# Optimization experiments

Measured on AMD Instinct MI355X. Metric: run time of the kernel, lower is better.

The kernel has to match this reference:

```python
import jax, jax.numpy as jnp
import numpy as np
from jax import lax

E = 4      # n_experts
K = 2      # top_k
D = 1024   # d_model
B, S = 4, 4096


def setup_inputs() -> dict:
    key = jax.random.key(0)
    ks = jax.random.split(key, 9)
    sc = 1.0 / np.sqrt(D)
    x = jax.random.normal(ks[0], (B, S, D), dtype=jnp.float32)
    Wg = jax.random.normal(ks[1], (E, D, D), dtype=jnp.float32) * sc
    bg = jax.random.normal(ks[2], (E, D), dtype=jnp.float32) * sc
    Wv = jax.random.normal(ks[3], (E, D, D), dtype=jnp.float32) * sc
    bv = jax.random.normal(ks[4], (E, D), dtype=jnp.float32) * sc
    Wd = jax.random.normal(ks[5], (E, D, D), dtype=jnp.float32) * sc
    # decay_bias_init = 1.0 (torch init.constant_)
    bd = jnp.ones((E, D), dtype=jnp.float32)
    Wgate = jax.random.normal(ks[7], (E, D), dtype=jnp.float32) * sc
    return {"x": x, "Wg": Wg, "bg": bg, "Wv": Wv, "bv": bv,
            "Wd": Wd, "bd": bd, "Wgate": Wgate}


def reference(x, Wg, bg, Wv, bv, Wd, bd, Wgate):
    # Per-expert projections (torch Linear: y = x @ W.T + b; W is (out,in))
    g = jnp.einsum('bsd,eod->ebso', x, Wg) + bg[:, None, None, :]  # (E,B,S,D)
    v = jnp.einsum('bsd,eod->ebso', x, Wv) + bv[:, None, None, :]
    d = jnp.einsum('bsd,eod->ebso', x, Wd) + bd[:, None, None, :]
    x_scan = jax.nn.sigmoid(g) * jnp.tanh(v)
    a = 0.001 + 0.998 * jax.nn.sigmoid(d)

    # Causal linear RNN: h_t = a_t * h_{t-1} + x_t, vectorized over (E,B,D)
    xs = jnp.moveaxis(x_scan, 2, 0)  # (S,E,B,D)
    as_ = jnp.moveaxis(a, 2, 0)      # (S,E,B,D)

    def step(h, inp):
        a_t, x_t = inp
        h = a_t * h + x_t
        return h, h

    h0 = jnp.zeros((E, B, x.shape[-1]), dtype=x.dtype)
    _, outs = lax.scan(step, h0, (as_, xs))        # (S,E,B,D)
    expert_outs = jnp.transpose(outs, (2, 0, 3, 1))  # (B,S,D,E)

    # Router: top-k experts per token, softmax over selected logits
    gate_logits = jnp.einsum('bsd,ed->bse', x, Wgate)  # (B,S,E)
    top_vals, top_idx = lax.top_k(gate_logits, K)      # (B,S,K)
    weights = jax.nn.softmax(top_vals, axis=-1)        # (B,S,K)

    idx = jnp.broadcast_to(top_idx[:, :, None, :],
                           (x.shape[0], x.shape[1], x.shape[2], K))
    selected = jnp.take_along_axis(expert_outs, idx, axis=-1)  # (B,S,D,K)
    return (selected * weights[:, :, None, :]).sum(axis=-1)
```

## Files before the change

kernel.cpp:

```cpp
#include <hip/hip_runtime.h>

#define E_EXP 4
#define D_MODEL 1024
#define B_BATCH 4
#define S_SEQ 4096
#define NTOK (B_BATCH*S_SEQ)
#define CHUNK 32
#define NCHUNK (S_SEQ/CHUNK)

typedef float f4 __attribute__((ext_vector_type(4)));
typedef float f32x4 __attribute__((ext_vector_type(4)));
typedef short bf16x8 __attribute__((ext_vector_type(8)));

__device__ __forceinline__ unsigned short f2b(float f){
  union{float f;unsigned u;}v; v.f=f;
  unsigned r = v.u + 0x7fffu + ((v.u>>16)&1u);
  return (unsigned short)(r>>16);
}
__device__ __forceinline__ float b2f_lo(unsigned v){ union{unsigned u;float f;}x; x.u=v<<16; return x.f; }
__device__ __forceinline__ float b2f_hi(unsigned v){ union{unsigned u;float f;}x; x.u=v&0xffff0000u; return x.f; }

__device__ __forceinline__ void gload_lds16(const void* g, void* l){
  __builtin_amdgcn_global_load_lds(
      (const __attribute__((address_space(1))) void*)g,
      (__attribute__((address_space(3))) void*)l, 16, 0, 0);
}

__global__ __launch_bounds__(256) void cvt_bf16(const float* __restrict__ src,
                                                unsigned short* __restrict__ dst)
{
  size_t i = ((size_t)blockIdx.x*256 + threadIdx.x)*4;
  f4 v = *(const f4*)(src + i);
  ushort4 o; o.x=f2b(v[0]); o.y=f2b(v[1]); o.z=f2b(v[2]); o.w=f2b(v[3]);
  *(ushort4*)(dst + i) = o;
}

__global__ __launch_bounds__(256) void cvt_w3(const float* __restrict__ Wg,
                                              const float* __restrict__ Wv,
                                              const float* __restrict__ Wd,
                                              unsigned short* __restrict__ Wcat,
                                              int e0)
{
  const size_t DD = (size_t)D_MODEL*D_MODEL;
  size_t i4 = ((size_t)blockIdx.x*256 + threadIdx.x)*4;
  size_t le3m = i4 >> 20;
  size_t rem  = i4 & (DD-1);
  int mat = (int)(le3m % 3);
  int le  = (int)(le3m / 3);
  const float* src = (mat==0 ? Wg : (mat==1 ? Wv : Wd)) + (size_t)(e0+le)*DD + rem;
  f4 v = *(const f4*)src;
  ushort4 o; o.x=f2b(v[0]); o.y=f2b(v[1]); o.z=f2b(v[2]); o.w=f2b(v[3]);
  *(ushort4*)(Wcat + le3m*DD + rem) = o;
}

__global__ __launch_bounds__(256) void router_kernel(
    const float* __restrict__ x, const float* __restrict__ Wgate,
    float* __restrict__ wtok)
{
  int gtid = blockIdx.x*256 + threadIdx.x;
  int tok  = gtid >> 6;
  int lane = threadIdx.x & 63;
  const float* xr = x + (size_t)tok * D_MODEL;
  float acc0=0.f,acc1=0.f,acc2=0.f,acc3=0.f;
  for (int k=lane;k<D_MODEL;k+=64){
    float xv = xr[k];
    acc0 += xv*Wgate[0*D_MODEL+k];
    acc1 += xv*Wgate[1*D_MODEL+k];
    acc2 += xv*Wgate[2*D_MODEL+k];
    acc3 += xv*Wgate[3*D_MODEL+k];
  }
  #pragma unroll
  for (int off=32;off>0;off>>=1){
    acc0 += __shfl_down(acc0,off);
    acc1 += __shfl_down(acc1,off);
    acc2 += __shfl_down(acc2,off);
    acc3 += __shfl_down(acc3,off);
  }
  if (lane==0){
    float l[4]={acc0,acc1,acc2,acc3};
    int i1=0;
    #pragma unroll
    for(int e=1;e<4;e++) if (l[e]>l[i1]) i1=e;
    int i2=-1;
    #pragma unroll
    for(int e=0;e<4;e++){ if(e==i1) continue; if(i2<0||l[e]>l[i2]) i2=e; }
    float ex = __expf(l[i2]-l[i1]);
    float w1 = 1.f/(1.f+ex);
    float w2 = ex/(1.f+ex);
    float w[4]={0.f,0.f,0.f,0.f};
    w[i1]=w1; w[i2]=w2;
    float* wp = wtok + (size_t)tok*E_EXP;
    wp[0]=w[0]; wp[1]=w[1]; wp[2]=w[2]; wp[3]=w[3];
  }
}

#define BM2 256
#define BN2 256
#define BK2 64
#define NT2 (D_MODEL/BK2)

__global__ __launch_bounds__(512, 2) void gemm256(
    const unsigned short* __restrict__ A,
    const unsigned short* __restrict__ Wcat,
    unsigned short* __restrict__ gvd)
{
  __shared__ unsigned short sA[2][BM2][BK2];
  __shared__ unsigned short sB[2][BN2][BK2];
  const size_t DD = (size_t)D_MODEL*D_MODEL;
  const size_t ND = (size_t)NTOK*D_MODEL;

  const int le    = blockIdx.z;
  const int mbase = blockIdx.x*BM2;
  const int ntile = blockIdx.y;
  const int mat   = ntile>>2;
  const int nbase = (ntile&3)*BN2;

  const int tid  = threadIdx.x;
  const int wave = tid>>6, lane = tid&63;
  const int wm = wave>>2, wn = wave&3;
  const int l15 = lane&15;
  const int l8  = lane>>3;
  const int lc  = (lane&7) ^ l8;

  const unsigned short* Wmat = Wcat + ((size_t)le*3 + mat)*DD;
  const unsigned short* gA = A + (size_t)(mbase + wave*8 + l8)*D_MODEL + lc*8;
  const int bBw = (wave>>1)*64 + (wave&1)*8;
  const unsigned short* gB = Wmat + (size_t)(nbase + bBw + l8)*D_MODEL + lc*8;

  const int arow = wm*128 + l15;
  const int brow = wn*64  + l15;
  const int ach0 = (((lane>>4)    ) ^ (lane&7))*8;
  const int ach1 = (((lane>>4) + 4) ^ (lane&7))*8;

  f32x4 acc[8][4];
  #pragma unroll
  for (int i=0;i<8;i++)
    #pragma unroll
    for (int j=0;j<4;j++) acc[i][j] = 0;

  bf16x8 af[4][2], bfv[2][2];

#define STAGE_A2(slot,t,mh) do{ \
  gload_lds16(gA + (size_t)((mh)*64)*D_MODEL     + (t)*BK2, &sA[slot][(mh)*64 + wave*8][0]); \
  gload_lds16(gA + (size_t)(128+(mh)*64)*D_MODEL + (t)*BK2, &sA[slot][128+(mh)*64 + wave*8][0]); \
}while(0)
#define STAGE_B2(slot,t,nh) do{ \
  gload_lds16(gB + (size_t)((nh)*32)*D_MODEL    + (t)*BK2, &sB[slot][bBw + (nh)*32][0]); \
  gload_lds16(gB + (size_t)((nh)*32+16)*D_MODEL + (t)*BK2, &sB[slot][bBw + (nh)*32 + 16][0]); \
}while(0)
#define LOAD_A2(slot,mh) do{ \
  _Pragma("unroll") for (int _m=0;_m<4;++_m){ \
    af[_m][0] = *(const bf16x8*)&sA[slot][arow + ((mh)*4+_m)*16][ach0]; \
    af[_m][1] = *(const bf16x8*)&sA[slot][arow + ((mh)*4+_m)*16][ach1]; \
  } \
}while(0)
#define LOAD_B2(slot,nh) do{ \
  _Pragma("unroll") for (int _n=0;_n<2;++_n){ \
    bfv[_n][0] = *(const bf16x8*)&sB[slot][brow + ((nh)*2+_n)*16][ach0]; \
    bfv[_n][1] = *(const bf16x8*)&sB[slot][brow + ((nh)*2+_n)*16][ach1]; \
  } \
}while(0)
#define MQ2(mh,nh) do{ \
  _Pragma("unroll") for (int _m=0;_m<4;++_m) \
  _Pragma("unroll") for (int _n=0;_n<2;++_n) \
  _Pragma("unroll") for (int _k=0;_k<2;++_k) \
    acc[(mh)*4+_m][(nh)*2+_n] = __builtin_amdgcn_mfma_f32_16x16x32_bf16( \
        af[_m][_k], bfv[_n][_k], acc[(mh)*4+_m][(nh)*2+_n], 0,0,0); \
}while(0)
#define KC_LGKM0  asm volatile("s_waitcnt lgkmcnt(0)" ::: "memory")
#define KC_LGKM8  asm volatile("s_waitcnt lgkmcnt(8)" ::: "memory")
#define KC_VM4    asm volatile("s_waitcnt vmcnt(4)" ::: "memory")
#define BAR       __builtin_amdgcn_s_barrier()
#define PRIO1     __builtin_amdgcn_s_setprio(1)
#define PRIO0     __builtin_amdgcn_s_setprio(0)

#define WINDOW2(slot,oslot,T1,T2) do{ \
  LOAD_A2(slot,0); LOAD_B2(slot,0); \
  STAGE_A2(oslot,T1,1); STAGE_B2(oslot,T1,0); \
  KC_LGKM8; BAR; KC_LGKM0; \
  PRIO1; MQ2(0,0); PRIO0; BAR; \
  LOAD_B2(slot,1); \
  BAR; KC_LGKM0; \
  PRIO1; MQ2(0,1); PRIO0; BAR; \
  LOAD_A2(slot,1); \
  STAGE_A2(slot,T2,0); \
  BAR; KC_LGKM0; \
  PRIO1; MQ2(1,1); PRIO0; BAR; \
  LOAD_B2(slot,0); \
  STAGE_B2(slot,T2,1); \
  KC_VM4; BAR; KC_LGKM0; \
  PRIO1; MQ2(1,0); PRIO0; BAR; \
}while(0)

  STAGE_A2(0,0,0); STAGE_A2(0,0,1); STAGE_B2(0,0,0); STAGE_B2(0,0,1);
  STAGE_A2(1,1,0); STAGE_B2(1,1,1);
  KC_VM4; BAR;

  for (int tp=0; tp<NT2/2; ++tp){
    int ta = 2*tp+1;
    int tb = 2*tp+2; if (tb>=NT2) tb -= NT2;
    int tc = 2*tp+3; if (tc>=NT2) tc -= NT2;
    WINDOW2(0,1,ta,tb);
    WINDOW2(1,0,tb,tc);
  }

  asm volatile("s_waitcnt vmcnt(0)" ::: "memory");

  unsigned short* outp = gvd + ((size_t)le*3 + mat)*ND;
  const int me = mbase + wm*128;
  const int ne = nbase + wn*64;
  #pragma unroll
  for (int mi=0;mi<8;mi++){
    #pragma unroll
    for (int r=0;r<4;r++){
      int m = me + mi*16 + (lane>>4)*4 + r;
      size_t rowoff = (size_t)m*D_MODEL;
      #pragma unroll
      for (int ni=0;ni<4;ni++){
        int n = ne + ni*16 + l15;
        outp[rowoff+n] = f2b(acc[mi][ni][r]);
      }
    }
  }
}

__global__ __launch_bounds__(512) void scan_pass1(
    unsigned short* __restrict__ gvd,
    const float* __restrict__ bg, const float* __restrict__ bv, const float* __restrict__ bd,
    float* __restrict__ P, float* __restrict__ U, int e0)
{
  const size_t ND = (size_t)NTOK*D_MODEL;
  int blk = blockIdx.x;
  int c  = blk % NCHUNK;
  int b  = (blk / NCHUNK) % B_BATCH;
  int le = blk / (NCHUNK*B_BATCH);
  int d0 = threadIdx.x*2;
  int e  = e0 + le;

  float bg0 = bg[(size_t)e*D_MODEL+d0], bg1 = bg[(size_t)e*D_MODEL+d0+1];
  float bv0 = bv[(size_t)e*D_MODEL+d0], bv1 = bv[(size_t)e*D_MODEL+d0+1];
  float bd0 = bd[(size_t)e*D_MODEL+d0], bd1 = bd[(size_t)e*D_MODEL+d0+1];

  unsigned short* gp = gvd + (size_t)le*3*ND;
  size_t base = (((size_t)b)*S_SEQ + (size_t)c*CHUNK)*D_MODEL + d0;
  float h0=0.f,h1=0.f,p0=1.f,p1=1.f;
  for (int t=0;t<CHUNK;t++){
    unsigned gw = *(const unsigned*)(gp + base);
    unsigned vw = *(const unsigned*)(gp + ND + base);
    unsigned dw = *(const unsigned*)(gp + 2*ND + base);
    float g0 = b2f_lo(gw)+bg0, g1 = b2f_hi(gw)+bg1;
    float v0 = b2f_lo(vw)+bv0, v1 = b2f_hi(vw)+bv1;
    float dd0 = b2f_lo(dw)+bd0, dd1 = b2f_hi(dw)+bd1;
    float x0 = (1.f/(1.f+__expf(-g0))) * (1.f - 2.f/(__expf(2.f*v0)+1.f));
    float x1 = (1.f/(1.f+__expf(-g1))) * (1.f - 2.f/(__expf(2.f*v1)+1.f));
    float a0 = 0.001f + 0.998f/(1.f+__expf(-dd0));
    float a1 = 0.001f + 0.998f/(1.f+__expf(-dd1));
    h0 = a0*h0 + x0; h1 = a1*h1 + x1;
    p0 *= a0; p1 *= a1;
    unsigned xsw = (unsigned)f2b(x0) | ((unsigned)f2b(x1)<<16);
    unsigned aaw = (unsigned)f2b(a0) | ((unsigned)f2b(a1)<<16);
    *(unsigned*)(gp + base)        = xsw;
    *(unsigned*)(gp + 2*ND + base) = aaw;
    base += D_MODEL;
  }
  size_t sidx = (((size_t)(le*B_BATCH + b))*NCHUNK + c)*D_MODEL + d0;
  P[sidx]=p0; P[sidx+1]=p1;
  U[sidx]=h0; U[sidx+1]=h1;
}

__global__ __launch_bounds__(256) void scan_pass2(
    const float* __restrict__ P, const float* __restrict__ U, float* __restrict__ Hinit)
{
  int ch = blockIdx.x*256 + threadIdx.x;
  int d  = ch & (D_MODEL-1);
  int eb = ch >> 10;
  size_t base = (size_t)eb*NCHUNK*D_MODEL + d;
  float H=0.f;
  for (int c=0;c<NCHUNK;c++){
    size_t idx = base + (size_t)c*D_MODEL;
    Hinit[idx] = H;
    H = P[idx]*H + U[idx];
  }
}

template<int G, int FIRST>
__global__ __launch_bounds__(512) void scan_pass3(
    const unsigned short* __restrict__ gvd,
    const float* __restrict__ Hinit, const float* __restrict__ wtok,
    float* __restrict__ out, int e0)
{
  const size_t ND = (size_t)NTOK*D_MODEL;
  int blk = blockIdx.x;
  int c = blk % NCHUNK;
  int b = blk / NCHUNK;
  int d0 = threadIdx.x*2;
  float h[G][2];
  #pragma unroll
  for (int le=0; le<G; le++){
    size_t hi = (((size_t)(le*B_BATCH+b))*NCHUNK + c)*D_MODEL + d0;
    h[le][0]=Hinit[hi]; h[le][1]=Hinit[hi+1];
  }
  int s0 = c*CHUNK;
  for (int t=0;t<CHUNK;t++){
    size_t n = (size_t)b*S_SEQ + s0 + t;
    float o0=0.f, o1=0.f;
    #pragma unroll
    for (int le=0;le<G;le++){
      float w = wtok[n*E_EXP + e0 + le];
      size_t idx = (size_t)le*3*ND + n*D_MODEL + d0;
      unsigned xv = *(const unsigned*)(gvd + idx);
      unsigned av = *(const unsigned*)(gvd + 2*ND + idx);
      h[le][0] = b2f_lo(av)*h[le][0] + b2f_lo(xv);
      h[le][1] = b2f_hi(av)*h[le][1] + b2f_hi(xv);
      o0 += w*h[le][0];
      o1 += w*h[le][1];
    }
    float* op = out + n*D_MODEL + d0;
    if (FIRST){ op[0]=o0;  op[1]=o1;  }
    else      { op[0]+=o0; op[1]+=o1; }
  }
}

extern "C" void kernel_launch(void* const* d_in, const int* in_sizes, int n_in,
                              void* d_out, int out_size, void* d_ws, size_t ws_size,
                              hipStream_t stream)
{
  const float* x     = (const float*)d_in[0];
  const float* Wg    = (const float*)d_in[1];
  const float* bg    = (const float*)d_in[2];
  const float* Wv    = (const float*)d_in[3];
  const float* bv    = (const float*)d_in[4];
  const float* Wd    = (const float*)d_in[5];
  const float* bd    = (const float*)d_in[6];
  const float* Wgate = (const float*)d_in[7];
  float* out = (float*)d_out;

  const size_t DD        = (size_t)D_MODEL*D_MODEL;
  const size_t ND        = (size_t)NTOK*D_MODEL;
  const size_t wtok_b    = (size_t)NTOK*E_EXP*4;
  const size_t xbf_b     = ND*2;
  const size_t w_per_e   = 3*DD*2;
  const size_t gvd_per_e = 3*ND*2;
  const size_t st_per_e  = (size_t)B_BATCH*NCHUNK*D_MODEL*4;

  int G = 1;
  for (int g = 4; g >= 1; g >>= 1){
    size_t need = wtok_b + xbf_b + (size_t)g*(w_per_e + gvd_per_e + 3*st_per_e);
    if (need <= ws_size){ G = g; break; }
  }

  char* wsb = (char*)d_ws;
  size_t off = 0;
  float*          wtok = (float*)(wsb+off);          off += wtok_b;
  unsigned short* xbf  = (unsigned short*)(wsb+off); off += xbf_b;
  unsigned short* Wcat = (unsigned short*)(wsb+off); off += (size_t)G*w_per_e;
  unsigned short* gvd  = (unsigned short*)(wsb+off); off += (size_t)G*gvd_per_e;
  float*          P    = (float*)(wsb+off);          off += (size_t)G*st_per_e;
  float*          U    = (float*)(wsb+off);          off += (size_t)G*st_per_e;
  float*          Hi   = (float*)(wsb+off);

  cvt_bf16<<<(unsigned)(ND/1024), 256, 0, stream>>>(x, xbf);
  router_kernel<<<NTOK/4, 256, 0, stream>>>(x, Wgate, wtok);

  for (int e0=0; e0<E_EXP; e0+=G){
    cvt_w3<<<(unsigned)((size_t)G*3*DD/1024), 256, 0, stream>>>(Wg, Wv, Wd, Wcat, e0);

    dim3 gg(NTOK/BM2, 3*D_MODEL/BN2, G);
    gemm256<<<gg, 512, 0, stream>>>(xbf, Wcat, gvd);

    scan_pass1<<<G*B_BATCH*NCHUNK, 512, 0, stream>>>(gvd, bg, bv, bd, P, U, e0);
    scan_pass2<<<G*B_BATCH*D_MODEL/256, 256, 0, stream>>>(P, U, Hi);
    bool first = (e0 == 0);
    if (G==4)      scan_pass3<4,1><<<B_BATCH*NCHUNK, 512, 0, stream>>>(gvd, Hi, wtok, out, e0);
    else if (G==2){
      if (first) scan_pass3<2,1><<<B_BATCH*NCHUNK, 512, 0, stream>>>(gvd, Hi, wtok, out, e0);
      else       scan_pass3<2,0><<<B_BATCH*NCHUNK, 512, 0, stream>>>(gvd, Hi, wtok, out, e0);
    } else {
      if (first) scan_pass3<1,1><<<B_BATCH*NCHUNK, 512, 0, stream>>>(gvd, Hi, wtok, out, e0);
      else       scan_pass3<1,0><<<B_BATCH*NCHUNK, 512, 0, stream>>>(gvd, Hi, wtok, out, e0);
    }
  }
}
```

Measured before the change: 833.7 us.

## Remap GEMM waves to 4x2 grid with 64x128 per-wave tiles

Changes the wave layout in the 256x256 GEMM from 2x4 (128x64 per wave) to 4x2 (64x128 per wave). The A fragments are now loaded once per K-step and reused across four B quarters, and the staging order and vmcnt threshold are reworked to match. The aim is to cut LDS reads of A and rebalance the global-to-LDS staging. It also changes the order of load and wait relative to the barriers, which risks races if the vmcnt accounting is off.

```diff
diff --git a/kernel.cpp b/kernel.cpp
--- a/kernel.cpp
+++ b/kernel.cpp
@@ -117,7 +117,7 @@
 
   const int tid  = threadIdx.x;
   const int wave = tid>>6, lane = tid&63;
-  const int wm = wave>>2, wn = wave&3;
+  const int wm = wave>>1, wn = wave&1;
   const int l15 = lane&15;
   const int l8  = lane>>3;
   const int lc  = (lane&7) ^ l8;
@@ -127,16 +127,16 @@
   const int bBw = (wave>>1)*64 + (wave&1)*8;
   const unsigned short* gB = Wmat + (size_t)(nbase + bBw + l8)*D_MODEL + lc*8;
 
-  const int arow = wm*128 + l15;
-  const int brow = wn*64  + l15;
+  const int arow = wm*64  + l15;
+  const int brow = wn*128 + l15;
   const int ach0 = (((lane>>4)    ) ^ (lane&7))*8;
   const int ach1 = (((lane>>4) + 4) ^ (lane&7))*8;
 
-  f32x4 acc[8][4];
+  f32x4 acc[4][8];
   #pragma unroll
-  for (int i=0;i<8;i++)
-    #pragma unroll
-    for (int j=0;j<4;j++) acc[i][j] = 0;
+  for (int i=0;i<4;i++)
+    #pragma unroll
+    for (int j=0;j<8;j++) acc[i][j] = 0;
 
   bf16x8 af[4][2], bfv[2][2];
 
@@ -148,75 +148,75 @@
   gload_lds16(gB + (size_t)((nh)*32)*D_MODEL    + (t)*BK2, &sB[slot][bBw + (nh)*32][0]); \
   gload_lds16(gB + (size_t)((nh)*32+16)*D_MODEL + (t)*BK2, &sB[slot][bBw + (nh)*32 + 16][0]); \
 }while(0)
-#define LOAD_A2(slot,mh) do{ \
+#define LOAD_A_ALL(slot) do{ \
   _Pragma("unroll") for (int _m=0;_m<4;++_m){ \
-    af[_m][0] = *(const bf16x8*)&sA[slot][arow + ((mh)*4+_m)*16][ach0]; \
-    af[_m][1] = *(const bf16x8*)&sA[slot][arow + ((mh)*4+_m)*16][ach1]; \
+    af[_m][0] = *(const bf16x8*)&sA[slot][arow + _m*16][ach0]; \
+    af[_m][1] = *(const bf16x8*)&sA[slot][arow + _m*16][ach1]; \
   } \
 }while(0)
-#define LOAD_B2(slot,nh) do{ \
+#define LOAD_BQ(slot,q) do{ \
   _Pragma("unroll") for (int _n=0;_n<2;++_n){ \
-    bfv[_n][0] = *(const bf16x8*)&sB[slot][brow + ((nh)*2+_n)*16][ach0]; \
-    bfv[_n][1] = *(const bf16x8*)&sB[slot][brow + ((nh)*2+_n)*16][ach1]; \
+    bfv[_n][0] = *(const bf16x8*)&sB[slot][brow + (q)*32 + _n*16][ach0]; \
+    bfv[_n][1] = *(const bf16x8*)&sB[slot][brow + (q)*32 + _n*16][ach1]; \
   } \
 }while(0)
-#define MQ2(mh,nh) do{ \
+#define MQ3(q) do{ \
   _Pragma("unroll") for (int _m=0;_m<4;++_m) \
   _Pragma("unroll") for (int _n=0;_n<2;++_n) \
   _Pragma("unroll") for (int _k=0;_k<2;++_k) \
-    acc[(mh)*4+_m][(nh)*2+_n] = __builtin_amdgcn_mfma_f32_16x16x32_bf16( \
-        af[_m][_k], bfv[_n][_k], acc[(mh)*4+_m][(nh)*2+_n], 0,0,0); \
+    acc[_m][(q)*2+_n] = __builtin_amdgcn_mfma_f32_16x16x32_bf16( \
+        af[_m][_k], bfv[_n][_k], acc[_m][(q)*2+_n], 0,0,0); \
 }while(0)
 #define KC_LGKM0  asm volatile("s_waitcnt lgkmcnt(0)" ::: "memory")
 #define KC_LGKM8  asm volatile("s_waitcnt lgkmcnt(8)" ::: "memory")
-#define KC_VM4    asm volatile("s_waitcnt vmcnt(4)" ::: "memory")
+#define KC_VM6    asm volatile("s_waitcnt vmcnt(6)" ::: "memory")
 #define BAR       __builtin_amdgcn_s_barrier()
 #define PRIO1     __builtin_amdgcn_s_setprio(1)
 #define PRIO0     __builtin_amdgcn_s_setprio(0)
 
-#define WINDOW2(slot,oslot,T1,T2) do{ \
-  LOAD_A2(slot,0); LOAD_B2(slot,0); \
-  STAGE_A2(oslot,T1,1); STAGE_B2(oslot,T1,0); \
+#define WINDOW3(slot,oslot,T1,T2) do{ \
+  LOAD_A_ALL(slot); LOAD_BQ(slot,0); \
+  STAGE_B2(oslot,T1,1); \
   KC_LGKM8; BAR; KC_LGKM0; \
-  PRIO1; MQ2(0,0); PRIO0; BAR; \
-  LOAD_B2(slot,1); \
+  PRIO1; MQ3(0); PRIO0; BAR; \
+  LOAD_BQ(slot,1); \
+  STAGE_A2(slot,T2,0); STAGE_A2(slot,T2,1); \
   BAR; KC_LGKM0; \
-  PRIO1; MQ2(0,1); PRIO0; BAR; \
-  LOAD_A2(slot,1); \
-  STAGE_A2(slot,T2,0); \
+  PRIO1; MQ3(1); PRIO0; BAR; \
+  LOAD_BQ(slot,2); \
   BAR; KC_LGKM0; \
-  PRIO1; MQ2(1,1); PRIO0; BAR; \
-  LOAD_B2(slot,0); \
-  STAGE_B2(slot,T2,1); \
-  KC_VM4; BAR; KC_LGKM0; \
-  PRIO1; MQ2(1,0); PRIO0; BAR; \
+  PRIO1; MQ3(2); PRIO0; BAR; \
+  LOAD_BQ(slot,3); \
+  STAGE_B2(slot,T2,0); \
+  KC_VM6; BAR; KC_LGKM0; \
+  PRIO1; MQ3(3); PRIO0; BAR; \
 }while(0)
 
   STAGE_A2(0,0,0); STAGE_A2(0,0,1); STAGE_B2(0,0,0); STAGE_B2(0,0,1);
-  STAGE_A2(1,1,0); STAGE_B2(1,1,1);
-  KC_VM4; BAR;
+  STAGE_A2(1,1,0); STAGE_A2(1,1,1); STAGE_B2(1,1,0);
+  KC_VM6; BAR;
 
   for (int tp=0; tp<NT2/2; ++tp){
     int ta = 2*tp+1;
     int tb = 2*tp+2; if (tb>=NT2) tb -= NT2;
     int tc = 2*tp+3; if (tc>=NT2) tc -= NT2;
-    WINDOW2(0,1,ta,tb);
-    WINDOW2(1,0,tb,tc);
+    WINDOW3(0,1,ta,tb);
+    WINDOW3(1,0,tb,tc);
   }
 
   asm volatile("s_waitcnt vmcnt(0)" ::: "memory");
 
   unsigned short* outp = gvd + ((size_t)le*3 + mat)*ND;
-  const int me = mbase + wm*128;
-  const int ne = nbase + wn*64;
+  const int me = mbase + wm*64;
+  const int ne = nbase + wn*128;
   #pragma unroll
-  for (int mi=0;mi<8;mi++){
+  for (int mi=0;mi<4;mi++){
     #pragma unroll
     for (int r=0;r<4;r++){
       int m = me + mi*16 + (lane>>4)*4 + r;
       size_t rowoff = (size_t)m*D_MODEL;
       #pragma unroll
-      for (int ni=0;ni<4;ni++){
+      for (int ni=0;ni<8;ni++){
         int n = ne + ni*16 + l15;
         outp[rowoff+n] = f2b(acc[mi][ni][r]);
       }
```

Result: slower. 852.4 us (+2.2%).

## Fuse gate/value/decay GEMMs with activation epilogue into packed x/a output

Applied to the files above, without the earlier changes.

Each GEMM block now computes all three projections (g, v, d) for the same output tile in sequence, holding the packed g results in registers, then applies the bias, sigmoid·tanh and decay activation in the epilogue. It writes a single interleaved bf16 (x, a) word per element instead of three bf16 matrices. scan_pass1 no longer recomputes activations or rewrites x and a, and both scan passes read one 8-byte load per pair. This removes a large amount of intermediate HBM traffic. The costs are higher register pressure (the launch_bounds min-blocks hint is dropped, and pk adds 64 registers) and three times as much serial work per block on a grid that is a third the size.

```diff
diff --git a/kernel.cpp b/kernel.cpp
--- a/kernel.cpp
+++ b/kernel.cpp
@@ -99,10 +99,12 @@
 #define BK2 64
 #define NT2 (D_MODEL/BK2)
 
-__global__ __launch_bounds__(512, 2) void gemm256(
+__global__ __launch_bounds__(512) void gemm_fused(
     const unsigned short* __restrict__ A,
     const unsigned short* __restrict__ Wcat,
-    unsigned short* __restrict__ gvd)
+    const float* __restrict__ bg, const float* __restrict__ bv, const float* __restrict__ bd,
+    unsigned* __restrict__ gxa,
+    int e0)
 {
   __shared__ unsigned short sA[2][BM2][BK2];
   __shared__ unsigned short sB[2][BN2][BK2];
@@ -111,9 +113,8 @@
 
   const int le    = blockIdx.z;
   const int mbase = blockIdx.x*BM2;
-  const int ntile = blockIdx.y;
-  const int mat   = ntile>>2;
-  const int nbase = (ntile&3)*BN2;
+  const int nbase = blockIdx.y*BN2;
+  const int e     = e0 + le;
 
   const int tid  = threadIdx.x;
   const int wave = tid>>6, lane = tid&63;
@@ -122,10 +123,10 @@
   const int l8  = lane>>3;
   const int lc  = (lane&7) ^ l8;
 
-  const unsigned short* Wmat = Wcat + ((size_t)le*3 + mat)*DD;
-  const unsigned short* gA = A + (size_t)(mbase + wave*8 + l8)*D_MODEL + lc*8;
+  const unsigned short* gA  = A + (size_t)(mbase + wave*8 + l8)*D_MODEL + lc*8;
   const int bBw = (wave>>1)*64 + (wave&1)*8;
-  const unsigned short* gB = Wmat + (size_t)(nbase + bBw + l8)*D_MODEL + lc*8;
+  const unsigned short* gB0 = Wcat + (size_t)le*3*DD + (size_t)(nbase + bBw + l8)*D_MODEL + lc*8;
+  const unsigned short* gB  = gB0;
 
   const int arow = wm*128 + l15;
   const int brow = wn*64  + l15;
@@ -133,12 +134,8 @@
   const int ach1 = (((lane>>4) + 4) ^ (lane&7))*8;
 
   f32x4 acc[8][4];
-  #pragma unroll
-  for (int i=0;i<8;i++)
-    #pragma unroll
-    for (int j=0;j<4;j++) acc[i][j] = 0;
-
   bf16x8 af[4][2], bfv[2][2];
+  unsigned pk[8][4][2];
 
 #define STAGE_A2(slot,t,mh) do{ \
   gload_lds16(gA + (size_t)((mh)*64)*D_MODEL     + (t)*BK2, &sA[slot][(mh)*64 + wave*8][0]); \
@@ -192,42 +189,92 @@
   PRIO1; MQ2(1,0); PRIO0; BAR; \
 }while(0)
 
-  STAGE_A2(0,0,0); STAGE_A2(0,0,1); STAGE_B2(0,0,0); STAGE_B2(0,0,1);
-  STAGE_A2(1,1,0); STAGE_B2(1,1,1);
-  KC_VM4; BAR;
-
-  for (int tp=0; tp<NT2/2; ++tp){
-    int ta = 2*tp+1;
-    int tb = 2*tp+2; if (tb>=NT2) tb -= NT2;
-    int tc = 2*tp+3; if (tc>=NT2) tc -= NT2;
-    WINDOW2(0,1,ta,tb);
-    WINDOW2(1,0,tb,tc);
-  }
-
-  asm volatile("s_waitcnt vmcnt(0)" ::: "memory");
-
-  unsigned short* outp = gvd + ((size_t)le*3 + mat)*ND;
+#define RUN_MAT() do{ \
+  _Pragma("unroll") for (int _i=0;_i<8;_i++) \
+    _Pragma("unroll") for (int _j=0;_j<4;_j++) acc[_i][_j] = 0; \
+  STAGE_A2(0,0,0); STAGE_A2(0,0,1); STAGE_B2(0,0,0); STAGE_B2(0,0,1); \
+  STAGE_A2(1,1,0); STAGE_B2(1,1,1); \
+  KC_VM4; BAR; \
+  for (int tp=0; tp<NT2/2; ++tp){ \
+    int ta = 2*tp+1; \
+    int tb = 2*tp+2; if (tb>=NT2) tb -= NT2; \
+    int tc = 2*tp+3; if (tc>=NT2) tc -= NT2; \
+    WINDOW2(0,1,ta,tb); \
+    WINDOW2(1,0,tb,tc); \
+  } \
+  asm volatile("s_waitcnt vmcnt(0)" ::: "memory"); \
+}while(0)
+
+  const int ne = nbase + wn*64;
   const int me = mbase + wm*128;
-  const int ne = nbase + wn*64;
+
+  RUN_MAT();
   #pragma unroll
-  for (int mi=0;mi<8;mi++){
-    #pragma unroll
-    for (int r=0;r<4;r++){
-      int m = me + mi*16 + (lane>>4)*4 + r;
-      size_t rowoff = (size_t)m*D_MODEL;
+  for (int mi=0;mi<8;mi++)
+    #pragma unroll
+    for (int ni=0;ni<4;ni++)
       #pragma unroll
-      for (int ni=0;ni<4;ni++){
-        int n = ne + ni*16 + l15;
-        outp[rowoff+n] = f2b(acc[mi][ni][r]);
+      for (int j=0;j<2;j++)
+        pk[mi][ni][j] = (unsigned)f2b(acc[mi][ni][2*j]) | ((unsigned)f2b(acc[mi][ni][2*j+1])<<16);
+
+  gB = gB0 + DD;
+  RUN_MAT();
+  {
+    float bgv[4], bvv[4];
+    #pragma unroll
+    for (int ni=0;ni<4;ni++){
+      int n = ne + ni*16 + l15;
+      bgv[ni] = bg[(size_t)e*D_MODEL + n];
+      bvv[ni] = bv[(size_t)e*D_MODEL + n];
+    }
+    #pragma unroll
+    for (int mi=0;mi<8;mi++)
+      #pragma unroll
+      for (int ni=0;ni<4;ni++)
+        #pragma unroll
+        for (int j=0;j<2;j++){
+          unsigned w = pk[mi][ni][j];
+          float g0 = b2f_lo(w)+bgv[ni], g1 = b2f_hi(w)+bgv[ni];
+          float v0 = acc[mi][ni][2*j]+bvv[ni], v1 = acc[mi][ni][2*j+1]+bvv[ni];
+          float x0 = (1.f/(1.f+__expf(-g0))) * (1.f - 2.f/(__expf(2.f*v0)+1.f));
+          float x1 = (1.f/(1.f+__expf(-g1))) * (1.f - 2.f/(__expf(2.f*v1)+1.f));
+          pk[mi][ni][j] = (unsigned)f2b(x0) | ((unsigned)f2b(x1)<<16);
+        }
+  }
+
+  gB = gB0 + 2*DD;
+  RUN_MAT();
+  {
+    float bdv[4];
+    #pragma unroll
+    for (int ni=0;ni<4;ni++) bdv[ni] = bd[(size_t)e*D_MODEL + ne + ni*16 + l15];
+    unsigned* outp = gxa + (size_t)le*ND;
+    #pragma unroll
+    for (int mi=0;mi<8;mi++){
+      #pragma unroll
+      for (int j=0;j<2;j++){
+        int m0 = me + mi*16 + (lane>>4)*4 + 2*j;
+        size_t ro0 = (size_t)m0*D_MODEL;
+        size_t ro1 = ro0 + D_MODEL;
+        #pragma unroll
+        for (int ni=0;ni<4;ni++){
+          int n = ne + ni*16 + l15;
+          float d0v = acc[mi][ni][2*j]   + bdv[ni];
+          float d1v = acc[mi][ni][2*j+1] + bdv[ni];
+          float a0 = 0.001f + 0.998f/(1.f+__expf(-d0v));
+          float a1 = 0.001f + 0.998f/(1.f+__expf(-d1v));
+          unsigned w = pk[mi][ni][j];
+          outp[ro0+n] = (w & 0xffffu) | ((unsigned)f2b(a0)<<16);
+          outp[ro1+n] = (w >> 16)     | ((unsigned)f2b(a1)<<16);
+        }
       }
     }
   }
 }
 
 __global__ __launch_bounds__(512) void scan_pass1(
-    unsigned short* __restrict__ gvd,
-    const float* __restrict__ bg, const float* __restrict__ bv, const float* __restrict__ bd,
-    float* __restrict__ P, float* __restrict__ U, int e0)
+    const unsigned* __restrict__ gxa,
+    float* __restrict__ P, float* __restrict__ U)
 {
   const size_t ND = (size_t)NTOK*D_MODEL;
   int blk = blockIdx.x;
@@ -235,32 +282,16 @@
   int b  = (blk / NCHUNK) % B_BATCH;
   int le = blk / (NCHUNK*B_BATCH);
   int d0 = threadIdx.x*2;
-  int e  = e0 + le;
-
-  float bg0 = bg[(size_t)e*D_MODEL+d0], bg1 = bg[(size_t)e*D_MODEL+d0+1];
-  float bv0 = bv[(size_t)e*D_MODEL+d0], bv1 = bv[(size_t)e*D_MODEL+d0+1];
-  float bd0 = bd[(size_t)e*D_MODEL+d0], bd1 = bd[(size_t)e*D_MODEL+d0+1];
-
-  unsigned short* gp = gvd + (size_t)le*3*ND;
+
+  const unsigned* gp = gxa + (size_t)le*ND;
   size_t base = (((size_t)b)*S_SEQ + (size_t)c*CHUNK)*D_MODEL + d0;
   float h0=0.f,h1=0.f,p0=1.f,p1=1.f;
   for (int t=0;t<CHUNK;t++){
-    unsigned gw = *(const unsigned*)(gp + base);
-    unsigned vw = *(const unsigned*)(gp + ND + base);
-    unsigned dw = *(const unsigned*)(gp + 2*ND + base);
-    float g0 = b2f_lo(gw)+bg0, g1 = b2f_hi(gw)+bg1;
-    float v0 = b2f_lo(vw)+bv0, v1 = b2f_hi(vw)+bv1;
-    float dd0 = b2f_lo(dw)+bd0, dd1 = b2f_hi(dw)+bd1;
-    float x0 = (1.f/(1.f+__expf(-g0))) * (1.f - 2.f/(__expf(2.f*v0)+1.f));
-    float x1 = (1.f/(1.f+__expf(-g1))) * (1.f - 2.f/(__expf(2.f*v1)+1.f));
-    float a0 = 0.001f + 0.998f/(1.f+__expf(-dd0));
-    float a1 = 0.001f + 0.998f/(1.f+__expf(-dd1));
+    uint2 w = *(const uint2*)(gp + base);
+    float x0 = b2f_lo(w.x), a0 = b2f_hi(w.x);
+    float x1 = b2f_lo(w.y), a1 = b2f_hi(w.y);
     h0 = a0*h0 + x0; h1 = a1*h1 + x1;
     p0 *= a0; p1 *= a1;
-    unsigned xsw = (unsigned)f2b(x0) | ((unsigned)f2b(x1)<<16);
-    unsigned aaw = (unsigned)f2b(a0) | ((unsigned)f2b(a1)<<16);
-    *(unsigned*)(gp + base)        = xsw;
-    *(unsigned*)(gp + 2*ND + base) = aaw;
     base += D_MODEL;
   }
   size_t sidx = (((size_t)(le*B_BATCH + b))*NCHUNK + c)*D_MODEL + d0;
@@ -285,7 +316,7 @@
 
 template<int G, int FIRST>
 __global__ __launch_bounds__(512) void scan_pass3(
-    const unsigned short* __restrict__ gvd,
+    const unsigned* __restrict__ gxa,
     const float* __restrict__ Hinit, const float* __restrict__ wtok,
     float* __restrict__ out, int e0)
 {
@@ -307,11 +338,9 @@
     #pragma unroll
     for (int le=0;le<G;le++){
       float w = wtok[n*E_EXP + e0 + le];
-      size_t idx = (size_t)le*3*ND + n*D_MODEL + d0;
-      unsigned xv = *(const unsigned*)(gvd + idx);
-      unsigned av = *(const unsigned*)(gvd + 2*ND + idx);
-      h[le][0] = b2f_lo(av)*h[le][0] + b2f_lo(xv);
-      h[le][1] = b2f_hi(av)*h[le][1] + b2f_hi(xv);
+      uint2 wv = *(const uint2*)(gxa + (size_t)le*ND + n*D_MODEL + d0);
+      h[le][0] = b2f_hi(wv.x)*h[le][0] + b2f_lo(wv.x);
+      h[le][1] = b2f_hi(wv.y)*h[le][1] + b2f_lo(wv.y);
       o0 += w*h[le][0];
       o1 += w*h[le][1];
     }
@@ -340,12 +369,12 @@
   const size_t wtok_b    = (size_t)NTOK*E_EXP*4;
   const size_t xbf_b     = ND*2;
   const size_t w_per_e   = 3*DD*2;
-  const size_t gvd_per_e = 3*ND*2;
+  const size_t gxa_per_e = ND*4;
   const size_t st_per_e  = (size_t)B_BATCH*NCHUNK*D_MODEL*4;
 
   int G = 1;
   for (int g = 4; g >= 1; g >>= 1){
-    size_t need = wtok_b + xbf_b + (size_t)g*(w_per_e + gvd_per_e + 3*st_per_e);
+    size_t need = wtok_b + xbf_b + (size_t)g*(w_per_e + gxa_per_e + 3*st_per_e);
     if (need <= ws_size){ G = g; break; }
   }
 
@@ -354,7 +383,7 @@
   float*          wtok = (float*)(wsb+off);          off += wtok_b;
   unsigned short* xbf  = (unsigned short*)(wsb+off); off += xbf_b;
   unsigned short* Wcat = (unsigned short*)(wsb+off); off += (size_t)G*w_per_e;
-  unsigned short* gvd  = (unsigned short*)(wsb+off); off += (size_t)G*gvd_per_e;
+  unsigned*       gxa  = (unsigned*)(wsb+off);       off += (size_t)G*gxa_per_e;
   float*          P    = (float*)(wsb+off);          off += (size_t)G*st_per_e;
   float*          U    = (float*)(wsb+off);          off += (size_t)G*st_per_e;
   float*          Hi   = (float*)(wsb+off);
@@ -365,19 +394,19 @@
   for (int e0=0; e0<E_EXP; e0+=G){
     cvt_w3<<<(unsigned)((size_t)G*3*DD/1024), 256, 0, stream>>>(Wg, Wv, Wd, Wcat, e0);
 
-    dim3 gg(NTOK/BM2, 3*D_MODEL/BN2, G);
-    gemm256<<<gg, 512, 0, stream>>>(xbf, Wcat, gvd);
-
-    scan_pass1<<<G*B_BATCH*NCHUNK, 512, 0, stream>>>(gvd, bg, bv, bd, P, U, e0);
+    dim3 gg(NTOK/BM2, D_MODEL/BN2, G);
+    gemm_fused<<<gg, 512, 0, stream>>>(xbf, Wcat, bg, bv, bd, gxa, e0);
+
+    scan_pass1<<<G*B_BATCH*NCHUNK, 512, 0, stream>>>(gxa, P, U);
     scan_pass2<<<G*B_BATCH*D_MODEL/256, 256, 0, stream>>>(P, U, Hi);
     bool first = (e0 == 0);
-    if (G==4)      scan_pass3<4,1><<<B_BATCH*NCHUNK, 512, 0, stream>>>(gvd, Hi, wtok, out, e0);
+    if (G==4)      scan_pass3<4,1><<<B_BATCH*NCHUNK, 512, 0, stream>>>(gxa, Hi, wtok, out, e0);
     else if (G==2){
-      if (first) scan_pass3<2,1><<<B_BATCH*NCHUNK, 512, 0, stream>>>(gvd, Hi, wtok, out, e0);
-      else       scan_pass3<2,0><<<B_BATCH*NCHUNK, 512, 0, stream>>>(gvd, Hi, wtok, out, e0);
+      if (first) scan_pass3<2,1><<<B_BATCH*NCHUNK, 512, 0, stream>>>(gxa, Hi, wtok, out, e0);
+      else       scan_pass3<2,0><<<B_BATCH*NCHUNK, 512, 0, stream>>>(gxa, Hi, wtok, out, e0);
     } else {
-      if (first) scan_pass3<1,1><<<B_BATCH*NCHUNK, 512, 0, stream>>>(gvd, Hi, wtok, out, e0);
-      else       scan_pass3<1,0><<<B_BATCH*NCHUNK, 512, 0, stream>>>(gvd, Hi, wtok, out, e0);
+      if (first) scan_pass3<1,1><<<B_BATCH*NCHUNK, 512, 0, stream>>>(gxa, Hi, wtok, out, e0);
+      else       scan_pass3<1,0><<<B_BATCH*NCHUNK, 512, 0, stream>>>(gxa, Hi, wtok, out, e0);
     }
   }
 }
```

Measured after the change: 1.199 ms. 1.44x slower.
